# Kernel optimization log

Hardware: AMD Instinct MI355X
Metric: run time of the kernel (lower is better)

Reference implementation:

```python
import jax, jax.numpy as jnp
import numpy as np
from jax import lax

B, T, I, H, L = 64, 512, 256, 512, 2


def setup_inputs() -> dict:
    key = jax.random.key(0)
    ks = jax.random.split(key, 5)
    s_in = (6.0 / (H + I)) ** 0.5   # xavier-uniform-like scale
    s_hh = (6.0 / (H + H)) ** 0.5
    return {
        "x": jax.random.normal(ks[0], (B, T, I), jnp.float32),
        "h_0": jnp.zeros((L, B, H), jnp.float32),
        "W_ih_0": jax.random.normal(ks[1], (H, I), jnp.float32) * s_in,
        "W_hh_0": jax.random.normal(ks[2], (H, H), jnp.float32) * s_hh,
        "b_ih_0": jnp.zeros((H,), jnp.float32),
        "b_hh_0": jnp.zeros((H,), jnp.float32),
        "W_ih_1": jax.random.normal(ks[3], (H, H), jnp.float32) * s_hh,
        "W_hh_1": jax.random.normal(ks[4], (H, H), jnp.float32) * s_hh,
        "b_ih_1": jnp.zeros((H,), jnp.float32),
        "b_hh_1": jnp.zeros((H,), jnp.float32),
    }


def _rnn_layer(xs, h0, W_ih, W_hh, b_ih, b_hh):
    # Precompute the input-to-hidden projection for all timesteps at once
    # (same math as per-step F.linear, just batched): [B,T,H]
    xW = jnp.einsum('bti,hi->bth', xs, W_ih) + b_ih + b_hh

    def step(h, xw_t):  # h:[B,H], xw_t:[B,H]
        h_new = jnp.tanh(xw_t + h @ W_hh.T)
        return h_new, h_new

    h_last, ys = lax.scan(step, h0, jnp.swapaxes(xW, 0, 1))  # ys: [T,B,H]
    return jnp.swapaxes(ys, 0, 1), h_last


def reference(x, h_0, W_ih_0, W_hh_0, b_ih_0, b_hh_0,
              W_ih_1, W_hh_1, b_ih_1, b_hh_1):
    out0, h_n0 = _rnn_layer(x, h_0[0], W_ih_0, W_hh_0, b_ih_0, b_hh_0)
    out1, h_n1 = _rnn_layer(out0, h_0[1], W_ih_1, W_hh_1, b_ih_1, b_hh_1)
    h_n = jnp.stack([h_n0, h_n1], axis=0)  # [L,B,H]
    return out1, h_n
```

## Files before the change

kernel.cpp:

```cpp
#include <hip/hip_runtime.h>


#define kB 64
#define kT 512
#define kI 256
#define kH 512
#define kBH (kB * kH)

typedef _Float16 half8 __attribute__((ext_vector_type(8)));
typedef float floatx4 __attribute__((ext_vector_type(4)));
typedef unsigned u32x2 __attribute__((ext_vector_type(2)));

#define MFMA(a, b, c) __builtin_amdgcn_mfma_f32_16x16x32_f16(a, b, c, 0, 0, 0)

constexpr size_t W16_B   = 0;
constexpr size_t WH0_B   = 1u * 1024 * 1024;
constexpr size_t WI1_B   = WH0_B + 512u * 1024;
constexpr size_t WH1_B   = WI1_B + 512u * 1024;
constexpr size_t OUT0M_B = 16u * 1024 * 1024;
constexpr size_t H1M_B   = OUT0M_B + (size_t)(kT + 1) * kBH * 2;
constexpr size_t CNT_B   = H1M_B + (size_t)(kT + 1) * kBH * 2;

__device__ inline void agent_store8(void* p, u32x2 v) {
    asm volatile("global_store_dwordx2 %0, %1, off sc1" :: "v"(p), "v"(v) : "memory");
}
__device__ inline int aload(const int* p) {
    return __hip_atomic_load(p, __ATOMIC_RELAXED, __HIP_MEMORY_SCOPE_AGENT);
}
__device__ inline void wait_slot(const int* p, int target) {
    int g = 0;
    while (aload(p) < target) if (++g > 100000000) break;
    asm volatile("" ::: "memory");
}
__device__ inline void wait_pair(const int* f, int target) {
    const int* p = f + (threadIdx.x & 1) * 32;
    int g = 0;
    for (;;) { int v = aload(p); if (__all(v >= target)) break; if (++g > 100000000) break; }
    asm volatile("" ::: "memory");
}
__device__ inline void wait_quad(const int* f, int own, int target) {
    const int idx = threadIdx.x & 3;
    const int* p = f + idx * 32;
    int g = 0;
    for (;;) {
        int v = (idx == own) ? target : aload(p);
        if (__all(v >= target)) break;
        if (++g > 100000000) break;
    }
    asm volatile("" ::: "memory");
}

__device__ inline float fast_tanh(float x) {
    float e = __expf(2.f * x);
    return 1.f - 2.f / (e + 1.f);
}

__device__ inline half8 cvt8(const float* p) {
    const float4* p4 = (const float4*)p;
    float4 a = p4[0], b = p4[1];
    half8 h;
    h[0] = (_Float16)a.x; h[1] = (_Float16)a.y; h[2] = (_Float16)a.z; h[3] = (_Float16)a.w;
    h[4] = (_Float16)b.x; h[5] = (_Float16)b.y; h[6] = (_Float16)b.z; h[7] = (_Float16)b.w;
    return h;
}

__global__ void setup_kernel(const float* __restrict__ h0,
                             const float* __restrict__ wih0, const float* __restrict__ whh0,
                             const float* __restrict__ wih1, const float* __restrict__ whh1,
                             _Float16* __restrict__ w16, _Float16* __restrict__ wh0_16,
                             _Float16* __restrict__ wi1_16, _Float16* __restrict__ wh1_16,
                             _Float16* __restrict__ out0m, _Float16* __restrict__ h1m,
                             int* __restrict__ cnt) {
    size_t tid = (size_t)blockIdx.x * blockDim.x + threadIdx.x;
    size_t stride = (size_t)gridDim.x * blockDim.x;
    for (size_t i = tid; i < (size_t)kH * kI; i += stride) w16[i] = (_Float16)wih0[i];
    for (size_t i = tid; i < (size_t)kH * kH; i += stride) {
        wh0_16[i] = (_Float16)whh0[i];
        wi1_16[i] = (_Float16)wih1[i];
        wh1_16[i] = (_Float16)whh1[i];
    }
    for (size_t i = tid; i < kBH; i += stride) {
        out0m[i] = (_Float16)h0[i];
        h1m[i]   = (_Float16)h0[kBH + i];
    }
    if (tid < 1024) cnt[tid] = 0;
}

__global__ __launch_bounds__(256) void xw_kernel(
    const float* __restrict__ x, const _Float16* __restrict__ w16,
    const float* __restrict__ bih, const float* __restrict__ bhh, float* xw) {
    const int mb = blockIdx.x >> 3, nb = blockIdx.x & 7;
    const int wave = threadIdx.x >> 6, lane = threadIdx.x & 63;
    const int r = lane & 15, q = lane >> 4;
    const int m0 = mb * 64 + wave * 16;
    half8 a[8];
#pragma unroll
    for (int ko = 0; ko < 8; ++ko)
        a[ko] = cvt8(x + (size_t)(m0 + r) * kI + ko * 32 + q * 8);
#pragma unroll
    for (int ct = 0; ct < 4; ++ct) {
        const int cc = nb * 64 + ct * 16 + r;
        const float bias = bih[cc] + bhh[cc];
        floatx4 acc = {bias, bias, bias, bias};
#pragma unroll
        for (int ko = 0; ko < 8; ++ko) {
            half8 b = *(const half8*)(w16 + (size_t)cc * kI + ko * 32 + q * 8);
            acc = MFMA(a[ko], b, acc);
        }
#pragma unroll
        for (int j = 0; j < 4; ++j)
            xw[(size_t)(m0 + q * 4 + j) * kH + cc] = acc[j];
    }
}

__global__ __launch_bounds__(1024) void scan_kernel(
    const float* xw,
    _Float16* out0m, _Float16* h1m,
    float* out1,
    const _Float16* __restrict__ wh0_16,
    const _Float16* __restrict__ wi1_16, const _Float16* __restrict__ wh1_16,
    const float* __restrict__ bih1, const float* __restrict__ bhh1,
    int* cnt) {
    __shared__ __align__(16) char smem[45056];

    const int blk = blockIdx.x;
    const int tid = threadIdx.x;
    const int wave = tid >> 6, lane = tid & 63;
    const int r = lane & 15, q = lane >> 4;
    const int rb = (r << 10), swz = (r & 7) << 4;
    const int rr = lane >> 2, cg = lane & 3;

    if (blk < 8) {
        const int g = blk >> 1, hf = blk & 1;
        const int b0 = g * 16;
        const int cc = hf * 256 + wave * 16 + r;
        half8 wfh[16];
#pragma unroll
        for (int ks = 0; ks < 16; ++ks)
            wfh[ks] = *(const half8*)(wh0_16 + (size_t)cc * kH + ks * 32 + q * 8);
        int* myf = cnt + (g * 2 + hf) * 32;
        const int* pef = cnt + (g * 2 + (hf ^ 1)) * 32;
        const int srow = tid >> 6, sunit = tid & 63;
        const size_t sg_off = (size_t)(b0 + srow) * kH + sunit * 8;
        char* sdst = smem + (((srow << 10) | (sunit << 4)) ^ ((srow & 7) << 4));
        char* ts = smem + 16384 + wave * 512;
        _Float16* st = out0m + (size_t)kBH + (size_t)(b0 + rr) * kH
                       + hf * 256 + wave * 16 + cg * 4;

        for (int t = 0; t < kT; ++t) {
            float xwv[4];
#pragma unroll
            for (int j = 0; j < 4; ++j)
                xwv[j] = xw[((size_t)(b0 + q * 4 + j) * kT + t) * kH + cc];
            if (t > 0) wait_slot(pef, t);
            *(half8*)sdst = *(const half8*)(out0m + (size_t)t * kBH + sg_off);
            __syncthreads();
            floatx4 acc = {0.f, 0.f, 0.f, 0.f};
#pragma unroll
            for (int ks = 0; ks < 16; ++ks) {
                half8 la = *(const half8*)(smem + ((rb | (ks << 6) | (q << 4)) ^ swz));
                acc = MFMA(la, wfh[ks], acc);
            }
#pragma unroll
            for (int j = 0; j < 4; ++j) {
                float v = fast_tanh(acc[j] + xwv[j]);
                *(_Float16*)(ts + (q * 4 + j) * 32 + r * 2) = (_Float16)v;
            }
            asm volatile("s_waitcnt lgkmcnt(0)" ::: "memory");
            u32x2 tv = *(const u32x2*)(ts + rr * 32 + cg * 8);
            agent_store8(st, tv);
            asm volatile("" ::: "memory");
            __builtin_amdgcn_s_waitcnt(0x0F70);
            __syncthreads();
            if (tid == 0)
                __hip_atomic_store(myf, t + 1, __ATOMIC_RELAXED, __HIP_MEMORY_SCOPE_AGENT);
            st += kBH;
        }
    } else {
        const int b2 = blk - 8;
        const int g = b2 >> 2, qb = b2 & 3;
        const int b0 = g * 16;
        const int ct = wave >> 1, part = wave & 1;
        const int cc = qb * 128 + ct * 16 + r;
        half8 wf[16];
        const _Float16* wsrc = part ? wi1_16 : wh1_16;
#pragma unroll
        for (int ks = 0; ks < 16; ++ks)
            wf[ks] = *(const half8*)(wsrc + (size_t)cc * kH + ks * 32 + q * 8);
        const float bias = (part == 0) ? (bih1[cc] + bhh1[cc]) : 0.f;
        int* myf = cnt + (8 + g * 4 + qb) * 32;
        const int* qf = cnt + (8 + g * 4) * 32;
        const int* lf = cnt + (g * 2) * 32;
        const int u = ct * 64 + lane;
        const int srow = u >> 5, sunit = u & 31;
        const size_t sg_off = (size_t)(b0 + srow) * kH + sunit * 16;
        const int tbase = part ? 16384 : 0;
        char* sd0 = smem + tbase + (((srow << 10) | (sunit << 5)) ^ ((srow & 7) << 4));
        char* sd1 = smem + tbase + ((((srow << 10) | (sunit << 5)) | 16) ^ ((srow & 7) << 4));
        float* redp = (float*)(smem + 32768) + (ct * 256 + lane * 4);
        char* tsp = smem + 40960 + ct * 512;
        _Float16* hst = h1m + (size_t)kBH + (size_t)(b0 + rr) * kH
                        + qb * 128 + ct * 16 + cg * 4;
        float* o1 = out1 + (size_t)(b0 + q * 4) * kT * kH + cc;

        for (int t = 0; t < kT; ++t) {
            const _Float16* sl;
            if (part == 0) {
                if (t > 0) wait_quad(qf, qb, t);
                sl = h1m + (size_t)t * kBH;
            } else {
                wait_pair(lf, t + 1);
                sl = out0m + (size_t)(t + 1) * kBH;
            }
            half8 s0 = *(const half8*)(sl + sg_off);
            half8 s1 = *(const half8*)(sl + sg_off + 8);
            *(half8*)sd0 = s0;
            *(half8*)sd1 = s1;
            __syncthreads();
            floatx4 acc = {0.f, 0.f, 0.f, 0.f};
            const char* tb = smem + tbase;
#pragma unroll
            for (int ks = 0; ks < 16; ++ks) {
                half8 la = *(const half8*)(tb + ((rb | (ks << 6) | (q << 4)) ^ swz));
                acc = MFMA(la, wf[ks], acc);
            }
            if (part == 1) *(floatx4*)redp = acc;
            __syncthreads();
            float vj[4];
            if (part == 0) {
                floatx4 o = *(const floatx4*)redp;
#pragma unroll
                for (int j = 0; j < 4; ++j) {
                    vj[j] = fast_tanh(acc[j] + o[j] + bias);
                    *(_Float16*)(tsp + (q * 4 + j) * 32 + r * 2) = (_Float16)vj[j];
                }
                asm volatile("s_waitcnt lgkmcnt(0)" ::: "memory");
                u32x2 tv = *(const u32x2*)(tsp + rr * 32 + cg * 8);
                agent_store8(hst, tv);
            }
            asm volatile("" ::: "memory");
            __builtin_amdgcn_s_waitcnt(0x0F70);
            __syncthreads();
            if (tid == 0)
                __hip_atomic_store(myf, t + 1, __ATOMIC_RELAXED, __HIP_MEMORY_SCOPE_AGENT);
            if (part == 0) {
#pragma unroll
                for (int j = 0; j < 4; ++j)
                    o1[(size_t)j * kT * kH + (size_t)t * kH] = vj[j];
            }
            hst += kBH;
        }
    }
}

__global__ void finalize_kernel(const _Float16* __restrict__ out0m,
                                const _Float16* __restrict__ h1m,
                                float* __restrict__ out) {
    int idx = blockIdx.x * blockDim.x + threadIdx.x;
    float* hn = out + (size_t)kB * kT * kH;
    if (idx < kBH) hn[idx] = (float)out0m[(size_t)kT * kBH + idx];
    else hn[idx] = (float)h1m[(size_t)kT * kBH + (idx - kBH)];
}

extern "C" void kernel_launch(void* const* d_in, const int* in_sizes, int n_in,
                              void* d_out, int out_size, void* d_ws, size_t ws_size,
                              hipStream_t stream) {
    const float* x    = (const float*)d_in[0];
    const float* h0in = (const float*)d_in[1];
    const float* wih0 = (const float*)d_in[2];
    const float* whh0 = (const float*)d_in[3];
    const float* bih0 = (const float*)d_in[4];
    const float* bhh0 = (const float*)d_in[5];
    const float* wih1 = (const float*)d_in[6];
    const float* whh1 = (const float*)d_in[7];
    const float* bih1 = (const float*)d_in[8];
    const float* bhh1 = (const float*)d_in[9];
    float* out = (float*)d_out;
    char* ws = (char*)d_ws;

    _Float16* w16    = (_Float16*)(ws + W16_B);
    _Float16* wh0_16 = (_Float16*)(ws + WH0_B);
    _Float16* wi1_16 = (_Float16*)(ws + WI1_B);
    _Float16* wh1_16 = (_Float16*)(ws + WH1_B);
    _Float16* out0m  = (_Float16*)(ws + OUT0M_B);
    _Float16* h1m    = (_Float16*)(ws + H1M_B);
    int* cnt         = (int*)(ws + CNT_B);

    setup_kernel<<<2048, 256, 0, stream>>>(h0in, wih0, whh0, wih1, whh1,
                                           w16, wh0_16, wi1_16, wh1_16, out0m, h1m, cnt);
    xw_kernel<<<4096, 256, 0, stream>>>(x, w16, bih0, bhh0, out);
    scan_kernel<<<24, 1024, 0, stream>>>(out, out0m, h1m, out,
                                         wh0_16, wi1_16, wh1_16, bih1, bhh1, cnt);
    finalize_kernel<<<256, 256, 0, stream>>>(out0m, h1m, out);
}
```

Baseline: 1.978 ms.

## Replace flag counters with sentinel-filled hidden-state buffers polled directly

The per-block atomic step counters are removed. Instead, setup pre-fills all future hidden-state slots with an all-ones (NaN) sentinel, and consumers spin on LLC-coherent loads of the data itself until no sentinel remains. This drops the post-store waitcnt, the extra barrier and the flag publish from every timestep. The layer-0 LDS staging buffer is double-buffered so the trailing barrier can go. The cost is a large sentinel fill in setup, plus a correctness risk if a genuine fp16 value ever matches the sentinel pattern or stores become visible partially.

New measurement: 2.210 ms. 11.7% more time.

```diff
diff --git a/kernel.cpp b/kernel.cpp
--- a/kernel.cpp
+++ b/kernel.cpp
@@ -9,6 +9,7 @@
 
 typedef _Float16 half8 __attribute__((ext_vector_type(8)));
 typedef float floatx4 __attribute__((ext_vector_type(4)));
+typedef unsigned u32x4 __attribute__((ext_vector_type(4)));
 typedef unsigned u32x2 __attribute__((ext_vector_type(2)));
 
 #define MFMA(a, b, c) __builtin_amdgcn_mfma_f32_16x16x32_f16(a, b, c, 0, 0, 0)
@@ -19,35 +20,18 @@
 constexpr size_t WH1_B   = WI1_B + 512u * 1024;
 constexpr size_t OUT0M_B = 16u * 1024 * 1024;
 constexpr size_t H1M_B   = OUT0M_B + (size_t)(kT + 1) * kBH * 2;
-constexpr size_t CNT_B   = H1M_B + (size_t)(kT + 1) * kBH * 2;
 
 __device__ inline void agent_store8(void* p, u32x2 v) {
     asm volatile("global_store_dwordx2 %0, %1, off sc1" :: "v"(p), "v"(v) : "memory");
 }
-__device__ inline int aload(const int* p) {
-    return __hip_atomic_load(p, __ATOMIC_RELAXED, __HIP_MEMORY_SCOPE_AGENT);
-}
-__device__ inline void wait_slot(const int* p, int target) {
-    int g = 0;
-    while (aload(p) < target) if (++g > 100000000) break;
-    asm volatile("" ::: "memory");
-}
-__device__ inline void wait_pair(const int* f, int target) {
-    const int* p = f + (threadIdx.x & 1) * 32;
-    int g = 0;
-    for (;;) { int v = aload(p); if (__all(v >= target)) break; if (++g > 100000000) break; }
-    asm volatile("" ::: "memory");
-}
-__device__ inline void wait_quad(const int* f, int own, int target) {
-    const int idx = threadIdx.x & 3;
-    const int* p = f + idx * 32;
-    int g = 0;
-    for (;;) {
-        int v = (idx == own) ? target : aload(p);
-        if (__all(v >= target)) break;
-        if (++g > 100000000) break;
-    }
-    asm volatile("" ::: "memory");
+#define LLC_LOAD16(dst, p) \
+    asm volatile("global_load_dwordx4 %0, %1, off sc1" : "=v"(dst) : "v"(p))
+
+__device__ inline unsigned dirty4(u32x4 v) {
+    unsigned m01 = v[0] > v[1] ? v[0] : v[1];
+    unsigned m23 = v[2] > v[3] ? v[2] : v[3];
+    unsigned m = m01 > m23 ? m01 : m23;
+    return m == 0xFFFFFFFFu;
 }
 
 __device__ inline float fast_tanh(float x) {
@@ -69,8 +53,7 @@
                              const float* __restrict__ wih1, const float* __restrict__ whh1,
                              _Float16* __restrict__ w16, _Float16* __restrict__ wh0_16,
                              _Float16* __restrict__ wi1_16, _Float16* __restrict__ wh1_16,
-                             _Float16* __restrict__ out0m, _Float16* __restrict__ h1m,
-                             int* __restrict__ cnt) {
+                             _Float16* __restrict__ out0m, _Float16* __restrict__ h1m) {
     size_t tid = (size_t)blockIdx.x * blockDim.x + threadIdx.x;
     size_t stride = (size_t)gridDim.x * blockDim.x;
     for (size_t i = tid; i < (size_t)kH * kI; i += stride) w16[i] = (_Float16)wih0[i];
@@ -83,7 +66,11 @@
         out0m[i] = (_Float16)h0[i];
         h1m[i]   = (_Float16)h0[kBH + i];
     }
-    if (tid < 1024) cnt[tid] = 0;
+    u32x4 s = {0xFFFFFFFFu, 0xFFFFFFFFu, 0xFFFFFFFFu, 0xFFFFFFFFu};
+    u32x4* a = (u32x4*)(out0m + kBH);
+    u32x4* b = (u32x4*)(h1m + kBH);
+    const size_t nf = (size_t)kT * kBH / 8;
+    for (size_t i = tid; i < nf; i += stride) { a[i] = s; b[i] = s; }
 }
 
 __global__ __launch_bounds__(256) void xw_kernel(
@@ -119,8 +106,7 @@
     float* out1,
     const _Float16* __restrict__ wh0_16,
     const _Float16* __restrict__ wi1_16, const _Float16* __restrict__ wh1_16,
-    const float* __restrict__ bih1, const float* __restrict__ bhh1,
-    int* cnt) {
+    const float* __restrict__ bih1, const float* __restrict__ bhh1) {
     __shared__ __align__(16) char smem[45056];
 
     const int blk = blockIdx.x;
@@ -138,27 +124,37 @@
 #pragma unroll
         for (int ks = 0; ks < 16; ++ks)
             wfh[ks] = *(const half8*)(wh0_16 + (size_t)cc * kH + ks * 32 + q * 8);
-        int* myf = cnt + (g * 2 + hf) * 32;
-        const int* pef = cnt + (g * 2 + (hf ^ 1)) * 32;
         const int srow = tid >> 6, sunit = tid & 63;
         const size_t sg_off = (size_t)(b0 + srow) * kH + sunit * 8;
-        char* sdst = smem + (((srow << 10) | (sunit << 4)) ^ ((srow & 7) << 4));
-        char* ts = smem + 16384 + wave * 512;
+        const int sdoff = ((srow << 10) | (sunit << 4)) ^ ((srow & 7) << 4);
+        char* ts = smem + 32768 + wave * 512;
         _Float16* st = out0m + (size_t)kBH + (size_t)(b0 + rr) * kH
                        + hf * 256 + wave * 16 + cg * 4;
 
         for (int t = 0; t < kT; ++t) {
+            char* bufS = (t & 1) ? smem + 16384 : smem;
             float xwv[4];
 #pragma unroll
             for (int j = 0; j < 4; ++j)
                 xwv[j] = xw[((size_t)(b0 + q * 4 + j) * kT + t) * kH + cc];
-            if (t > 0) wait_slot(pef, t);
-            *(half8*)sdst = *(const half8*)(out0m + (size_t)t * kBH + sg_off);
+            u32x4 sv;
+            {
+                const _Float16* sgp = out0m + (size_t)t * kBH + sg_off;
+                int guard = 0;
+                for (;;) {
+                    LLC_LOAD16(sv, sgp);
+                    __builtin_amdgcn_s_waitcnt(0x0F70);
+                    __builtin_amdgcn_sched_barrier(0);
+                    if (!__any(dirty4(sv))) break;
+                    if (++guard > (1 << 22)) break;
+                }
+            }
+            *(u32x4*)(bufS + sdoff) = sv;
             __syncthreads();
             floatx4 acc = {0.f, 0.f, 0.f, 0.f};
 #pragma unroll
             for (int ks = 0; ks < 16; ++ks) {
-                half8 la = *(const half8*)(smem + ((rb | (ks << 6) | (q << 4)) ^ swz));
+                half8 la = *(const half8*)(bufS + ((rb | (ks << 6) | (q << 4)) ^ swz));
                 acc = MFMA(la, wfh[ks], acc);
             }
 #pragma unroll
@@ -169,11 +165,6 @@
             asm volatile("s_waitcnt lgkmcnt(0)" ::: "memory");
             u32x2 tv = *(const u32x2*)(ts + rr * 32 + cg * 8);
             agent_store8(st, tv);
-            asm volatile("" ::: "memory");
-            __builtin_amdgcn_s_waitcnt(0x0F70);
-            __syncthreads();
-            if (tid == 0)
-                __hip_atomic_store(myf, t + 1, __ATOMIC_RELAXED, __HIP_MEMORY_SCOPE_AGENT);
             st += kBH;
         }
     } else {
@@ -188,9 +179,6 @@
         for (int ks = 0; ks < 16; ++ks)
             wf[ks] = *(const half8*)(wsrc + (size_t)cc * kH + ks * 32 + q * 8);
         const float bias = (part == 0) ? (bih1[cc] + bhh1[cc]) : 0.f;
-        int* myf = cnt + (8 + g * 4 + qb) * 32;
-        const int* qf = cnt + (8 + g * 4) * 32;
-        const int* lf = cnt + (g * 2) * 32;
         const int u = ct * 64 + lane;
         const int srow = u >> 5, sunit = u & 31;
         const size_t sg_off = (size_t)(b0 + srow) * kH + sunit * 16;
@@ -204,18 +192,23 @@
         float* o1 = out1 + (size_t)(b0 + q * 4) * kT * kH + cc;
 
         for (int t = 0; t < kT; ++t) {
-            const _Float16* sl;
-            if (part == 0) {
-                if (t > 0) wait_quad(qf, qb, t);
-                sl = h1m + (size_t)t * kBH;
-            } else {
-                wait_pair(lf, t + 1);
-                sl = out0m + (size_t)(t + 1) * kBH;
-            }
-            half8 s0 = *(const half8*)(sl + sg_off);
-            half8 s1 = *(const half8*)(sl + sg_off + 8);
-            *(half8*)sd0 = s0;
-            *(half8*)sd1 = s1;
+            const _Float16* sl = (part == 0) ? h1m + (size_t)t * kBH
+                                             : out0m + (size_t)(t + 1) * kBH;
+            const _Float16* base = sl + sg_off;
+            u32x4 s0, s1;
+            {
+                int guard = 0;
+                for (;;) {
+                    LLC_LOAD16(s0, base);
+                    LLC_LOAD16(s1, base + 8);
+                    __builtin_amdgcn_s_waitcnt(0x0F70);
+                    __builtin_amdgcn_sched_barrier(0);
+                    if (!__any(dirty4(s0) | dirty4(s1))) break;
+                    if (++guard > (1 << 22)) break;
+                }
+            }
+            *(u32x4*)sd0 = s0;
+            *(u32x4*)sd1 = s1;
             __syncthreads();
             floatx4 acc = {0.f, 0.f, 0.f, 0.f};
             const char* tb = smem + tbase;
@@ -226,9 +219,9 @@
             }
             if (part == 1) *(floatx4*)redp = acc;
             __syncthreads();
-            float vj[4];
             if (part == 0) {
                 floatx4 o = *(const floatx4*)redp;
+                float vj[4];
 #pragma unroll
                 for (int j = 0; j < 4; ++j) {
                     vj[j] = fast_tanh(acc[j] + o[j] + bias);
@@ -237,13 +230,6 @@
                 asm volatile("s_waitcnt lgkmcnt(0)" ::: "memory");
                 u32x2 tv = *(const u32x2*)(tsp + rr * 32 + cg * 8);
                 agent_store8(hst, tv);
-            }
-            asm volatile("" ::: "memory");
-            __builtin_amdgcn_s_waitcnt(0x0F70);
-            __syncthreads();
-            if (tid == 0)
-                __hip_atomic_store(myf, t + 1, __ATOMIC_RELAXED, __HIP_MEMORY_SCOPE_AGENT);
-            if (part == 0) {
 #pragma unroll
                 for (int j = 0; j < 4; ++j)
                     o1[(size_t)j * kT * kH + (size_t)t * kH] = vj[j];
@@ -284,12 +270,11 @@
     _Float16* wh1_16 = (_Float16*)(ws + WH1_B);
     _Float16* out0m  = (_Float16*)(ws + OUT0M_B);
     _Float16* h1m    = (_Float16*)(ws + H1M_B);
-    int* cnt         = (int*)(ws + CNT_B);
 
     setup_kernel<<<2048, 256, 0, stream>>>(h0in, wih0, whh0, wih1, whh1,
-                                           w16, wh0_16, wi1_16, wh1_16, out0m, h1m, cnt);
+                                           w16, wh0_16, wi1_16, wh1_16, out0m, h1m);
     xw_kernel<<<4096, 256, 0, stream>>>(x, w16, bih0, bhh0, out);
     scan_kernel<<<24, 1024, 0, stream>>>(out, out0m, h1m, out,
-                                         wh0_16, wi1_16, wh1_16, bih1, bhh1, cnt);
+                                         wh0_16, wi1_16, wh1_16, bih1, bhh1);
     finalize_kernel<<<256, 256, 0, stream>>>(out0m, h1m, out);
 }
```

## Keep own hidden slice in LDS and overlap own-half MFMAs with peer wait

Applied to the files above, without the earlier changes.

Each scan block now writes its freshly computed hidden-state slice directly into a double-buffered LDS copy. It computes the MFMA contribution from its own columns before waiting on peer blocks, and only fetches the peer blocks' slices from global memory after the flag wait. This shortens the critical path of each recurrent step by moving part of the matmul ahead of the cross-block synchronization and by cutting global reads. It costs more LDS (double buffer) and more complex indexing, and the part==0 waves of layer 1 do more work than the part==1 waves.

Result: slower. 4.395 ms (+122.2%).

```diff
diff --git a/kernel.cpp b/kernel.cpp
--- a/kernel.cpp
+++ b/kernel.cpp
@@ -9,6 +9,7 @@
 
 typedef _Float16 half8 __attribute__((ext_vector_type(8)));
 typedef float floatx4 __attribute__((ext_vector_type(4)));
+typedef unsigned u32x4 __attribute__((ext_vector_type(4)));
 typedef unsigned u32x2 __attribute__((ext_vector_type(2)));
 
 #define MFMA(a, b, c) __builtin_amdgcn_mfma_f32_16x16x32_f16(a, b, c, 0, 0, 0)
@@ -121,50 +122,74 @@
     const _Float16* __restrict__ wi1_16, const _Float16* __restrict__ wh1_16,
     const float* __restrict__ bih1, const float* __restrict__ bhh1,
     int* cnt) {
-    __shared__ __align__(16) char smem[45056];
+    __shared__ __align__(16) char smem[61440];
 
     const int blk = blockIdx.x;
     const int tid = threadIdx.x;
     const int wave = tid >> 6, lane = tid & 63;
     const int r = lane & 15, q = lane >> 4;
-    const int rb = (r << 10), swz = (r & 7) << 4;
+    const int rb = r << 10, swz = (r & 7) << 4;
     const int rr = lane >> 2, cg = lane & 3;
+    const int srow = tid >> 6, sunit = tid & 63;
+    const int sdoff = ((srow << 10) | (sunit << 4)) ^ ((srow & 7) << 4);
 
     if (blk < 8) {
         const int g = blk >> 1, hf = blk & 1;
         const int b0 = g * 16;
         const int cc = hf * 256 + wave * 16 + r;
-        half8 wfh[16];
-#pragma unroll
-        for (int ks = 0; ks < 16; ++ks)
-            wfh[ks] = *(const half8*)(wh0_16 + (size_t)cc * kH + ks * 32 + q * 8);
+        const _Float16* wrow = wh0_16 + (size_t)cc * kH;
+        half8 wfOwn[8], wfPeer[8];
+#pragma unroll
+        for (int i = 0; i < 8; ++i) {
+            wfOwn[i]  = *(const half8*)(wrow + hf * 256 + i * 32 + q * 8);
+            wfPeer[i] = *(const half8*)(wrow + (hf ^ 1) * 256 + i * 32 + q * 8);
+        }
         int* myf = cnt + (g * 2 + hf) * 32;
         const int* pef = cnt + (g * 2 + (hf ^ 1)) * 32;
-        const int srow = tid >> 6, sunit = tid & 63;
-        const size_t sg_off = (size_t)(b0 + srow) * kH + sunit * 8;
-        char* sdst = smem + (((srow << 10) | (sunit << 4)) ^ ((srow & 7) << 4));
-        char* ts = smem + 16384 + wave * 512;
+        char* ts = smem + 32768 + wave * 512;
         _Float16* st = out0m + (size_t)kBH + (size_t)(b0 + rr) * kH
                        + hf * 256 + wave * 16 + cg * 4;
+        const size_t pg_off = (size_t)(b0 + srow) * kH + (hf ^ 1) * 256 + sunit * 4;
+        const int pdoff = (srow << 10) + ((((hf ^ 1) << 9) | (sunit << 3))
+                                          ^ ((srow & 7) << 4));
+        {
+            u32x4 v = *(const u32x4*)(out0m + (size_t)(b0 + srow) * kH + sunit * 8);
+            *(u32x4*)(smem + sdoff) = v;
+        }
+        __syncthreads();
 
         for (int t = 0; t < kT; ++t) {
+            char* HR = smem + (t & 1) * 16384;
+            char* HW = smem + ((t + 1) & 1) * 16384;
             float xwv[4];
 #pragma unroll
             for (int j = 0; j < 4; ++j)
                 xwv[j] = xw[((size_t)(b0 + q * 4 + j) * kT + t) * kH + cc];
-            if (t > 0) wait_slot(pef, t);
-            *(half8*)sdst = *(const half8*)(out0m + (size_t)t * kBH + sg_off);
-            __syncthreads();
             floatx4 acc = {0.f, 0.f, 0.f, 0.f};
 #pragma unroll
-            for (int ks = 0; ks < 16; ++ks) {
-                half8 la = *(const half8*)(smem + ((rb | (ks << 6) | (q << 4)) ^ swz));
-                acc = MFMA(la, wfh[ks], acc);
+            for (int i = 0; i < 8; ++i) {
+                const int ks = hf * 8 + i;
+                half8 la = *(const half8*)(HR + ((rb | (ks << 6) | (q << 4)) ^ swz));
+                acc = MFMA(la, wfOwn[i], acc);
+            }
+            if (t > 0) {
+                wait_slot(pef, t);
+                u32x2 pv = *(const u32x2*)(out0m + (size_t)t * kBH + pg_off);
+                *(u32x2*)(HR + pdoff) = pv;
+            }
+            __syncthreads();
+#pragma unroll
+            for (int i = 0; i < 8; ++i) {
+                const int ks = (hf ^ 1) * 8 + i;
+                half8 la = *(const half8*)(HR + ((rb | (ks << 6) | (q << 4)) ^ swz));
+                acc = MFMA(la, wfPeer[i], acc);
             }
 #pragma unroll
             for (int j = 0; j < 4; ++j) {
                 float v = fast_tanh(acc[j] + xwv[j]);
-                *(_Float16*)(ts + (q * 4 + j) * 32 + r * 2) = (_Float16)v;
+                const int row = q * 4 + j;
+                *(_Float16*)(ts + row * 32 + r * 2) = (_Float16)v;
+                *(_Float16*)(HW + (row << 10) + ((cc * 2) ^ ((row & 7) << 4))) = (_Float16)v;
             }
             asm volatile("s_waitcnt lgkmcnt(0)" ::: "memory");
             u32x2 tv = *(const u32x2*)(ts + rr * 32 + cg * 8);
@@ -182,49 +207,98 @@
         const int b0 = g * 16;
         const int ct = wave >> 1, part = wave & 1;
         const int cc = qb * 128 + ct * 16 + r;
-        half8 wf[16];
-        const _Float16* wsrc = part ? wi1_16 : wh1_16;
-#pragma unroll
-        for (int ks = 0; ks < 16; ++ks)
-            wf[ks] = *(const half8*)(wsrc + (size_t)cc * kH + ks * 32 + q * 8);
+        half8 wfOwnQ[4], wfPeerQ[12], wfi[16];
+        if (part == 0) {
+#pragma unroll
+            for (int i = 0; i < 4; ++i)
+                wfOwnQ[i] = *(const half8*)(wh1_16 + (size_t)cc * kH
+                                            + (qb * 4 + i) * 32 + q * 8);
+#pragma unroll
+            for (int i = 0; i < 12; ++i) {
+                const int ks = i + (i >= qb * 4 ? 4 : 0);
+                wfPeerQ[i] = *(const half8*)(wh1_16 + (size_t)cc * kH + ks * 32 + q * 8);
+            }
+        } else {
+#pragma unroll
+            for (int ks = 0; ks < 16; ++ks)
+                wfi[ks] = *(const half8*)(wi1_16 + (size_t)cc * kH + ks * 32 + q * 8);
+        }
         const float bias = (part == 0) ? (bih1[cc] + bhh1[cc]) : 0.f;
         int* myf = cnt + (8 + g * 4 + qb) * 32;
         const int* qf = cnt + (8 + g * 4) * 32;
         const int* lf = cnt + (g * 2) * 32;
-        const int u = ct * 64 + lane;
-        const int srow = u >> 5, sunit = u & 31;
-        const size_t sg_off = (size_t)(b0 + srow) * kH + sunit * 16;
-        const int tbase = part ? 16384 : 0;
-        char* sd0 = smem + tbase + (((srow << 10) | (sunit << 5)) ^ ((srow & 7) << 4));
-        char* sd1 = smem + tbase + ((((srow << 10) | (sunit << 5)) | 16) ^ ((srow & 7) << 4));
-        float* redp = (float*)(smem + 32768) + (ct * 256 + lane * 4);
-        char* tsp = smem + 40960 + ct * 512;
+        char* Ob = smem + 32768;
+        float* redp = (float*)(smem + 49152) + (ct * 256 + lane * 4);
+        char* tsp = smem + 57344 + ct * 512;
         _Float16* hst = h1m + (size_t)kBH + (size_t)(b0 + rr) * kH
                         + qb * 128 + ct * 16 + cg * 4;
         float* o1 = out1 + (size_t)(b0 + q * 4) * kT * kH + cc;
+        const int s1 = ct * 64 + lane;
+        int prow3[3], pc3[3];
+#pragma unroll
+        for (int k3 = 0; k3 < 3; ++k3) {
+            const int u = s1 + k3 * 512;
+            const int row = u / 96, w = u % 96;
+            prow3[k3] = row;
+            pc3[k3] = w * 4 + (w * 4 >= qb * 128 ? 128 : 0);
+        }
+        const int u1 = ct * 64 + lane;
+        const int osrow = u1 >> 5, osunit = u1 & 31;
+        const size_t og_off = (size_t)(b0 + osrow) * kH + osunit * 16;
+        char* od0 = Ob + (((osrow << 10) | (osunit << 5)) ^ ((osrow & 7) << 4));
+        char* od1 = Ob + ((((osrow << 10) | (osunit << 5)) | 16) ^ ((osrow & 7) << 4));
+
+        {
+            u32x4 v = *(const u32x4*)(h1m + (size_t)(b0 + srow) * kH + sunit * 8);
+            *(u32x4*)(smem + sdoff) = v;
+        }
+        __syncthreads();
 
         for (int t = 0; t < kT; ++t) {
-            const _Float16* sl;
+            char* HR = smem + (t & 1) * 16384;
+            char* HW = smem + ((t + 1) & 1) * 16384;
+            floatx4 acc = {0.f, 0.f, 0.f, 0.f};
             if (part == 0) {
-                if (t > 0) wait_quad(qf, qb, t);
-                sl = h1m + (size_t)t * kBH;
+#pragma unroll
+                for (int i = 0; i < 4; ++i) {
+                    const int ks = qb * 4 + i;
+                    half8 la = *(const half8*)(HR + ((rb | (ks << 6) | (q << 4)) ^ swz));
+                    acc = MFMA(la, wfOwnQ[i], acc);
+                }
+                if (t > 0) {
+                    wait_quad(qf, qb, t);
+#pragma unroll
+                    for (int k3 = 0; k3 < 3; ++k3) {
+                        u32x2 pv = *(const u32x2*)(h1m + (size_t)t * kBH
+                                     + (size_t)(b0 + prow3[k3]) * kH + pc3[k3]);
+                        *(u32x2*)(HR + (prow3[k3] << 10)
+                                  + ((pc3[k3] * 2) ^ ((prow3[k3] & 7) << 4))) = pv;
+                    }
+                }
             } else {
                 wait_pair(lf, t + 1);
-                sl = out0m + (size_t)(t + 1) * kBH;
-            }
-            half8 s0 = *(const half8*)(sl + sg_off);
-            half8 s1 = *(const half8*)(sl + sg_off + 8);
-            *(half8*)sd0 = s0;
-            *(half8*)sd1 = s1;
-            __syncthreads();
-            floatx4 acc = {0.f, 0.f, 0.f, 0.f};
-            const char* tb = smem + tbase;
-#pragma unroll
-            for (int ks = 0; ks < 16; ++ks) {
-                half8 la = *(const half8*)(tb + ((rb | (ks << 6) | (q << 4)) ^ swz));
-                acc = MFMA(la, wf[ks], acc);
-            }
-            if (part == 1) *(floatx4*)redp = acc;
+                const _Float16* sl = out0m + (size_t)(t + 1) * kBH;
+                half8 s0 = *(const half8*)(sl + og_off);
+                half8 s1v = *(const half8*)(sl + og_off + 8);
+                *(half8*)od0 = s0;
+                *(half8*)od1 = s1v;
+            }
+            __syncthreads();
+            if (part == 0) {
+#pragma unroll
+                for (int i = 0; i < 12; ++i) {
+                    const int ks = i + (i >= qb * 4 ? 4 : 0);
+                    half8 la = *(const half8*)(HR + ((rb | (ks << 6) | (q << 4)) ^ swz));
+                    acc = MFMA(la, wfPeerQ[i], acc);
+                }
+            } else {
+#pragma unroll
+                for (int ks = 0; ks < 16; ++ks) {
+                    half8 la = *(const half8*)(Ob + ((rb | (ks << 6) | (q << 4)) ^ swz));
+                    acc = MFMA(la, wfi[ks], acc);
+                }
+                *(floatx4*)redp = acc;
+            }
             __syncthreads();
             float vj[4];
             if (part == 0) {
@@ -232,7 +306,10 @@
 #pragma unroll
                 for (int j = 0; j < 4; ++j) {
                     vj[j] = fast_tanh(acc[j] + o[j] + bias);
-                    *(_Float16*)(tsp + (q * 4 + j) * 32 + r * 2) = (_Float16)vj[j];
+                    const int row = q * 4 + j;
+                    *(_Float16*)(tsp + row * 32 + r * 2) = (_Float16)vj[j];
+                    *(_Float16*)(HW + (row << 10) + ((cc * 2) ^ ((row & 7) << 4)))
+                        = (_Float16)vj[j];
                 }
                 asm volatile("s_waitcnt lgkmcnt(0)" ::: "memory");
                 u32x2 tv = *(const u32x2*)(tsp + rr * 32 + cg * 8);
```
